# Kernel optimization log

Hardware: AMD Instinct MI355X
Metric: run time of the kernel (lower is better)

The kernel has to match this reference:

```python
import jax, jax.numpy as jnp
import numpy as np

N, E, ET, C, H, L = 100000, 500000, 3, 128, 128, 3
LN_EPS = 1e-5
L2_EPS = 1e-12


def setup_inputs() -> dict:
    ks = jax.random.split(jax.random.key(0), 12)
    s = 0.05
    return {
        "x": jax.random.normal(ks[0], (N, C), jnp.float32),
        "edges": jax.random.randint(ks[1], (ET, 2, E), 0, N),
        "Wp": jax.random.normal(ks[2], (ET, C, C), jnp.float32) * s,
        "bp": jax.random.normal(ks[3], (ET, C), jnp.float32) * s,
        "Wl0": jax.random.normal(ks[4], (ET, C, H), jnp.float32) * s,
        "bl0": jax.random.normal(ks[5], (ET, H), jnp.float32) * s,
        "Wr0": jax.random.normal(ks[6], (ET, C, H), jnp.float32) * s,
        "Wl": jax.random.normal(ks[7], (L - 1, ET, H, H), jnp.float32) * s,
        "bl": jax.random.normal(ks[8], (L - 1, ET, H), jnp.float32) * s,
        "Wr": jax.random.normal(ks[9], (L - 1, ET, H, H), jnp.float32) * s,
        "ln_g": jnp.ones((L - 1, H), jnp.float32),
        "ln_b": jnp.zeros((L - 1, H), jnp.float32),
    }


def _mean_aggr(msg, dst, n):
    # scatter-mean of per-edge messages onto destination nodes
    summed = jax.ops.segment_sum(msg, dst, num_segments=n)
    deg = jax.ops.segment_sum(jnp.ones((dst.shape[0],), msg.dtype), dst, num_segments=n)
    return summed / jnp.maximum(deg, 1.0)[:, None]


def _sage(h, ei, Wl_, bl_, Wr_, Wp_=None, bp_=None, normalize=False):
    # PyG SAGEConv: out = lin_l(mean_{j in N(i)} h_j) + lin_r(h_i)
    src, dst = ei[0], ei[1]
    hs = jax.nn.relu(h @ Wp_ + bp_) if Wp_ is not None else h  # project=True path
    agg = _mean_aggr(hs[src], dst, h.shape[0])
    out = agg @ Wl_ + bl_ + h @ Wr_
    if normalize:
        out = out / jnp.maximum(jnp.linalg.norm(out, axis=-1, keepdims=True), L2_EPS)
    return out


def _layer_norm(h, g, b):
    mu = h.mean(-1, keepdims=True)
    var = ((h - mu) ** 2).mean(-1, keepdims=True)
    return (h - mu) / jnp.sqrt(var + LN_EPS) * g + b


def _forward(x, edges, Wp, bp, Wl0, bl0, Wr0, Wl, bl, Wr, ln_g, ln_b):
    et = edges.shape[0]
    # layer 0: project=True, normalize=True; HeteroConv mean over edge types
    h = sum(_sage(x, edges[t], Wl0[t], bl0[t], Wr0[t], Wp[t], bp[t], True)
            for t in range(et)) / et
    h = _layer_norm(jax.nn.relu(h), ln_g[0], ln_b[0])  # dropout = identity (eval)
    n_rest = Wl.shape[0]
    for l in range(n_rest):
        h = sum(_sage(h, edges[t], Wl[l, t], bl[l, t], Wr[l, t])
                for t in range(et)) / et
        if l != n_rest - 1:
            h = _layer_norm(jax.nn.relu(h), ln_g[l + 1], ln_b[l + 1])
    return h


def reference(x, edges, Wp, bp, Wl0, bl0, Wr0, Wl, bl, Wr, ln_g, ln_b):
    return _forward(x, edges, Wp, bp, Wl0, bl0, Wr0, Wl, bl, Wr, ln_g, ln_b)
```

## Files before the change

### kernel.cpp

```cpp
#include <hip/hip_runtime.h>
#include <math.h>

#define CH 128
#define ETC 3
#define LN_EPS 1e-5f

typedef unsigned short u16;
typedef unsigned int u32;
typedef __attribute__((ext_vector_type(8))) short short8;
typedef __attribute__((ext_vector_type(4))) float f32x4;

__device__ __forceinline__ u16 f2bf(float f) {
    u32 u = __float_as_uint(f);
    u += 0x7FFFu + ((u >> 16) & 1u);
    return (u16)(u >> 16);
}
__device__ __forceinline__ float bflo(u32 u) { return __uint_as_float(u << 16); }
__device__ __forceinline__ float bfhi(u32 u) { return __uint_as_float(u & 0xFFFF0000u); }

__device__ __forceinline__ f32x4 mfma16(short8 a, short8 b, f32x4 c) {
    return __builtin_amdgcn_mfma_f32_16x16x32_bf16(a, b, c, 0, 0, 0);
}
__device__ __forceinline__ short8 ld8(const u16* p) { return *(const short8*)p; }

__global__ __launch_bounds__(256) void pack_w(
    const float* __restrict__ Wp, const float* __restrict__ Wl0,
    const float* __restrict__ Wr0, const float* __restrict__ Wl,
    const float* __restrict__ Wr, const float* __restrict__ bl,
    u16* __restrict__ Bswz, float* __restrict__ bls)
{
    if (blockIdx.x == 0) {
        int l = threadIdx.x >> 7, i = threadIdx.x & 127;
        bls[threadIdx.x] = (bl[((size_t)l * ETC + 0) * CH + i] +
                            bl[((size_t)l * ETC + 1) * CH + i] +
                            bl[((size_t)l * ETC + 2) * CH + i]) * (1.f / 3.f);
    }
    int grp = blockIdx.x * 256 + threadIdx.x;
    if (grp >= 17 * 2048) return;
    int lane = grp & 63;
    int t1 = grp >> 6;
    int nt = t1 & 7, t2 = t1 >> 3;
    int s = t2 & 3, mat = t2 >> 2;
    int q = lane >> 4, c = lane & 15;
    int nn = nt * 16 + c;

    const float* s0;
    const float* s1 = nullptr;
    const float* s2 = nullptr;
    float scale = 1.f;
    if (mat < 3) {
        s0 = Wp + (size_t)mat * CH * CH;
    } else if (mat < 9) {
        int t = (mat - 3) >> 1;
        s0 = ((mat - 3) & 1) ? Wr0 + (size_t)t * CH * CH : Wl0 + (size_t)t * CH * CH;
    } else {
        int l = (mat < 13) ? 0 : 1;
        int mm = mat - (l ? 13 : 9);
        scale = 1.f / 3.f;
        if (mm < 3) s0 = Wl + ((size_t)l * ETC + mm) * CH * CH;
        else {
            s0 = Wr + ((size_t)l * ETC + 0) * CH * CH;
            s1 = s0 + CH * CH;
            s2 = s1 + CH * CH;
        }
    }
    short8 o;
    #pragma unroll
    for (int j = 0; j < 8; ++j) {
        int k = s * 32 + q * 8 + j;
        float v = s0[(size_t)k * CH + nn];
        if (s1) v += s1[(size_t)k * CH + nn] + s2[(size_t)k * CH + nn];
        o[j] = (short)f2bf(v * scale);
    }
    *(short8*)&Bswz[(size_t)grp * 8] = o;
}

__global__ __launch_bounds__(256) void cast_x(
    const float* __restrict__ x, u16* __restrict__ xb, int total)
{
    int i = (blockIdx.x * 256 + threadIdx.x) * 8;
    if (i >= total) return;
    short8 o;
    #pragma unroll
    for (int j = 0; j < 8; ++j) o[j] = (short)f2bf(x[i + j]);
    *(short8*)&xb[i] = o;
}

template<int MODE>
__global__ __launch_bounds__(256, MODE == 0 ? 3 : 4) void combine_k(
    const u16* __restrict__ agg0, const u16* __restrict__ agg1,
    const u16* __restrict__ agg2, const u16* __restrict__ self,
    const u16* __restrict__ Bs, const float* __restrict__ bias,
    const float* __restrict__ lg, const float* __restrict__ lb,
    u16* __restrict__ outb, float* __restrict__ outf, int nrows)
{
    __shared__ __align__(16) u16 Bsh[CH * CH];
    const int tid = threadIdx.x;
    const int w = tid >> 6, lane = tid & 63;
    const int q = lane >> 4, c = lane & 15;
    const int rbase = (blockIdx.x * 4 + w) * 16;
    const int arow = rbase + c;
    constexpr int NM = (MODE == 0) ? 6 : ((MODE == 3) ? 1 : 4);
    constexpr int NA = (MODE == 3) ? 1 : 4;

    const u16* As[4];
    if constexpr (MODE == 3) {
        As[0] = self;
    } else {
        As[0] = agg0; As[1] = agg1; As[2] = agg2; As[3] = self;
    }

    short8 af[NA][4];
    #pragma unroll
    for (int a = 0; a < NA; ++a)
        #pragma unroll
        for (int s = 0; s < 4; ++s)
            af[a][s] = ld8(&As[a][(size_t)arow * CH + s * 32 + q * 8]);

    f32x4 acc[8] = {};
    f32x4 res[8] = {};

    #pragma unroll
    for (int m = 0; m < NM; ++m) {
        __syncthreads();
        const u16* bsrc = Bs + (size_t)m * CH * CH;
        #pragma unroll
        for (int i = 0; i < 8; ++i)
            *(short8*)&Bsh[(i * 256 + tid) * 8] = ld8(&bsrc[(i * 256 + tid) * 8]);
        __syncthreads();

        constexpr int AI_TBL0[6] = {0, 3, 1, 3, 2, 3};
        const int ai = (MODE == 0) ? AI_TBL0[m]
                     : (MODE == 3) ? 0
                     : ((m < 3) ? m : 3);

        #pragma unroll
        for (int s = 0; s < 4; ++s) {
            #pragma unroll
            for (int nt = 0; nt < 8; ++nt) {
                short8 bv = *(const short8*)&Bsh[((size_t)(s * 8 + nt) * 64 + lane) * 8];
                acc[nt] = mfma16(af[ai][s], bv, acc[nt]);
            }
        }

        if constexpr (MODE == 0) {
            if (m & 1) {
                const int t = m >> 1;
                float ss[4] = {0.f, 0.f, 0.f, 0.f};
                #pragma unroll
                for (int nt = 0; nt < 8; ++nt) {
                    float bf = bias[t * CH + nt * 16 + c];
                    #pragma unroll
                    for (int r = 0; r < 4; ++r) {
                        float v = acc[nt][r] + bf;
                        acc[nt][r] = v;
                        ss[r] += v * v;
                    }
                }
                #pragma unroll
                for (int msk = 1; msk < 16; msk <<= 1)
                    #pragma unroll
                    for (int r = 0; r < 4; ++r) ss[r] += __shfl_xor(ss[r], msk, 64);
                float sc[4];
                #pragma unroll
                for (int r = 0; r < 4; ++r)
                    sc[r] = 1.f / (3.f * fmaxf(sqrtf(ss[r]), 1e-12f));
                #pragma unroll
                for (int nt = 0; nt < 8; ++nt)
                    #pragma unroll
                    for (int r = 0; r < 4; ++r) {
                        res[nt][r] += acc[nt][r] * sc[r];
                        acc[nt][r] = 0.f;
                    }
            }
        }
    }

    if constexpr (MODE != 0) {
        #pragma unroll
        for (int nt = 0; nt < 8; ++nt) {
            float bv = bias[nt * 16 + c];
            #pragma unroll
            for (int r = 0; r < 4; ++r) res[nt][r] = acc[nt][r] + bv;
        }
    }

    if constexpr (MODE == 2) {
        #pragma unroll
        for (int nt = 0; nt < 8; ++nt)
            #pragma unroll
            for (int r = 0; r < 4; ++r) {
                int row = rbase + q * 4 + r;
                if (row < nrows) outf[(size_t)row * CH + nt * 16 + c] = res[nt][r];
            }
        return;
    }

    if constexpr (MODE == 3) {
        #pragma unroll
        for (int nt = 0; nt < 8; ++nt)
            #pragma unroll
            for (int r = 0; r < 4; ++r) {
                int row = rbase + q * 4 + r;
                outb[(size_t)row * CH + nt * 16 + c] = f2bf(fmaxf(res[nt][r], 0.f));
            }
        return;
    }

    {
        float s1[4] = {0.f, 0.f, 0.f, 0.f}, s2[4] = {0.f, 0.f, 0.f, 0.f};
        #pragma unroll
        for (int nt = 0; nt < 8; ++nt)
            #pragma unroll
            for (int r = 0; r < 4; ++r) {
                float v = fmaxf(res[nt][r], 0.f);
                res[nt][r] = v;
                s1[r] += v;
                s2[r] += v * v;
            }
        #pragma unroll
        for (int msk = 1; msk < 16; msk <<= 1)
            #pragma unroll
            for (int r = 0; r < 4; ++r) {
                s1[r] += __shfl_xor(s1[r], msk, 64);
                s2[r] += __shfl_xor(s2[r], msk, 64);
            }
        float mu[4], rs[4];
        #pragma unroll
        for (int r = 0; r < 4; ++r) {
            mu[r] = s1[r] * (1.f / 128.f);
            float var = s2[r] * (1.f / 128.f) - mu[r] * mu[r];
            rs[r] = rsqrtf(var + LN_EPS);
        }
        #pragma unroll
        for (int nt = 0; nt < 8; ++nt) {
            float gv = lg[nt * 16 + c], bv = lb[nt * 16 + c];
            #pragma unroll
            for (int r = 0; r < 4; ++r) {
                int row = rbase + q * 4 + r;
                outb[(size_t)row * CH + nt * 16 + c] =
                    f2bf((res[nt][r] - mu[r]) * rs[r] * gv + bv);
            }
        }
    }
}

__global__ __launch_bounds__(256) void agg_k(
    const u16* __restrict__ msg, const int* __restrict__ rowptr,
    const int* __restrict__ col, u16* __restrict__ agg, int n,
    int Ecap, unsigned long long aggstride)
{
    const int t = blockIdx.y;
    rowptr += (size_t)t * (n + 1);
    col += (size_t)t * Ecap;
    agg += (size_t)t * aggstride;

    int gid = blockIdx.x * 256 + threadIdx.x;
    int node = gid >> 5;
    int lane = threadIdx.x & 31;
    if (node >= n) return;
    int s = rowptr[node], e = rowptr[node + 1];
    const uint2* m64 = (const uint2*)msg;
    float a0 = 0.f, a1 = 0.f, a2 = 0.f, a3 = 0.f;
    float b0 = 0.f, b1 = 0.f, b2 = 0.f, b3 = 0.f;
    int j = s;
    for (; j + 2 <= e; j += 2) {
        int s0 = col[j], s1i = col[j + 1];
        uint2 v0 = m64[(size_t)s0 * 32 + lane];
        uint2 v1 = m64[(size_t)s1i * 32 + lane];
        a0 += bflo(v0.x); a1 += bfhi(v0.x); a2 += bflo(v0.y); a3 += bfhi(v0.y);
        b0 += bflo(v1.x); b1 += bfhi(v1.x); b2 += bflo(v1.y); b3 += bfhi(v1.y);
    }
    if (j < e) {
        int s0 = col[j];
        uint2 v0 = m64[(size_t)s0 * 32 + lane];
        a0 += bflo(v0.x); a1 += bfhi(v0.x); a2 += bflo(v0.y); a3 += bfhi(v0.y);
    }
    a0 += b0; a1 += b1; a2 += b2; a3 += b3;
    float inv = 1.f / (float)max(e - s, 1);
    uint2 o;
    o.x = (u32)f2bf(a0 * inv) | ((u32)f2bf(a1 * inv) << 16);
    o.y = (u32)f2bf(a2 * inv) | ((u32)f2bf(a3 * inv) << 16);
    ((uint2*)agg)[(size_t)node * 32 + lane] = o;
}

__global__ __launch_bounds__(256) void hist_k(
    const int* __restrict__ edges, int* __restrict__ cnt, int E, int n)
{
    int t = blockIdx.y;
    int e = blockIdx.x * 256 + threadIdx.x;
    if (e >= E) return;
    int dst = edges[(size_t)t * 2 * E + E + e];
    atomicAdd(&cnt[t * n + dst], 1);
}

__global__ __launch_bounds__(256) void scan1_k(
    const int* __restrict__ cnt, int* __restrict__ bsum, int n, int nbs)
{
    int t = blockIdx.y, b = blockIdx.x;
    int i = b * 256 + threadIdx.x;
    int v = (i < n) ? cnt[t * n + i] : 0;
    #pragma unroll
    for (int m = 1; m < 64; m <<= 1) v += __shfl_xor(v, m, 64);
    __shared__ int wsum[4];
    if ((threadIdx.x & 63) == 0) wsum[threadIdx.x >> 6] = v;
    __syncthreads();
    if (threadIdx.x == 0) bsum[t * nbs + b] = wsum[0] + wsum[1] + wsum[2] + wsum[3];
}

__global__ __launch_bounds__(512) void scan2_k(int* __restrict__ bsum, int nbs, int nb)
{
    int t = blockIdx.x;
    int tid = threadIdx.x;
    __shared__ int sh[512];
    int v = (tid < nb) ? bsum[t * nbs + tid] : 0;
    sh[tid] = v;
    __syncthreads();
    for (int off = 1; off < 512; off <<= 1) {
        int x = (tid >= off) ? sh[tid - off] : 0;
        __syncthreads();
        sh[tid] += x;
        __syncthreads();
    }
    if (tid < nb) bsum[t * nbs + tid] = sh[tid] - v;
}

__global__ __launch_bounds__(256) void scan3_k(
    const int* __restrict__ cnt, const int* __restrict__ bsum,
    int* __restrict__ rowptr, int n, int nbs)
{
    int t = blockIdx.y, b = blockIdx.x;
    int tid = threadIdx.x;
    int i = b * 256 + tid;
    __shared__ int sh[256];
    int v = (i < n) ? cnt[t * n + i] : 0;
    sh[tid] = v;
    __syncthreads();
    for (int off = 1; off < 256; off <<= 1) {
        int x = (tid >= off) ? sh[tid - off] : 0;
        __syncthreads();
        sh[tid] += x;
        __syncthreads();
    }
    int excl = sh[tid] - v + bsum[t * nbs + b];
    if (i < n) rowptr[(size_t)t * (n + 1) + i] = excl;
    if (i == n - 1) rowptr[(size_t)t * (n + 1) + n] = excl + v;
}

__global__ __launch_bounds__(256) void fill_k(
    const int* __restrict__ edges, const int* __restrict__ rowptr,
    int* __restrict__ cnt2, int* __restrict__ colbuf, int E, int n)
{
    int t = blockIdx.y;
    int e = blockIdx.x * 256 + threadIdx.x;
    if (e >= E) return;
    int src = edges[(size_t)t * 2 * E + e];
    int dst = edges[(size_t)t * 2 * E + E + e];
    int pos = rowptr[(size_t)t * (n + 1) + dst] + atomicAdd(&cnt2[t * n + dst], 1);
    colbuf[(size_t)t * E + pos] = src;
}

extern "C" void kernel_launch(void* const* d_in, const int* in_sizes, int n_in,
                              void* d_out, int out_size, void* d_ws, size_t ws_size,
                              hipStream_t stream) {
    const float* x    = (const float*)d_in[0];
    const int*   edges= (const int*)d_in[1];
    const float* Wp   = (const float*)d_in[2];
    const float* bp   = (const float*)d_in[3];
    const float* Wl0  = (const float*)d_in[4];
    const float* bl0  = (const float*)d_in[5];
    const float* Wr0  = (const float*)d_in[6];
    const float* Wl   = (const float*)d_in[7];
    const float* bl   = (const float*)d_in[8];
    const float* Wr   = (const float*)d_in[9];
    const float* ln_g = (const float*)d_in[10];
    const float* ln_b = (const float*)d_in[11];
    float* out = (float*)d_out;

    const int n  = in_sizes[0] / CH;
    const int E  = in_sizes[1] / (2 * ETC);
    const int npad = ((n + 255) / 256) * 256;
    const int NBS = 512;
    const int nb = (n + 255) / 256;
    const size_t MS = (size_t)CH * CH;

    char* p = (char*)d_ws;
    u16* xb   = (u16*)p;  p += (size_t)npad * CH * 2;
    u16* hs   = (u16*)p;  p += (size_t)npad * CH * 2;
    u16* agg  = (u16*)p;  p += (size_t)ETC * npad * CH * 2;
    u16* Bswz = (u16*)p;  p += 17 * MS * 2;
    float* bls = (float*)p; p += 256 * 4;
    int* cnt    = (int*)p;  p += (size_t)ETC * n * 4;
    int* rowptr = (int*)p;  p += (size_t)ETC * (n + 1) * 4;
    int* colbuf = (int*)p;  p += (size_t)ETC * E * 4;
    int* bsum   = (int*)p;

    const dim3 b256(256);
    const dim3 ge((E + 255) / 256, ETC);
    const dim3 gs(nb, ETC);
    const int gb = (n + 63) / 64;
    const int ga = (n * 32 + 255) / 256;

    hipMemsetAsync(cnt, 0, (size_t)ETC * n * sizeof(int), stream);
    hist_k<<<ge, b256, 0, stream>>>(edges, cnt, E, n);
    scan1_k<<<gs, b256, 0, stream>>>(cnt, bsum, n, NBS);
    scan2_k<<<ETC, 512, 0, stream>>>(bsum, NBS, nb);
    scan3_k<<<gs, b256, 0, stream>>>(cnt, bsum, rowptr, n, NBS);
    hipMemsetAsync(cnt, 0, (size_t)ETC * n * sizeof(int), stream);
    fill_k<<<ge, b256, 0, stream>>>(edges, rowptr, cnt, colbuf, E, n);

    pack_w<<<136, b256, 0, stream>>>(Wp, Wl0, Wr0, Wl, Wr, bl, Bswz, bls);
    cast_x<<<(n * CH / 8 + 255) / 256, b256, 0, stream>>>(x, xb, n * CH);

    for (int t = 0; t < ETC; ++t) {
        combine_k<3><<<gb, b256, 0, stream>>>(
            nullptr, nullptr, nullptr, xb, Bswz + (size_t)t * MS, bp + t * CH,
            nullptr, nullptr, hs, nullptr, n);
        agg_k<<<dim3(ga, 1), b256, 0, stream>>>(hs, rowptr + (size_t)t * (n + 1),
                                                colbuf + (size_t)t * E,
                                                agg + (size_t)t * npad * CH, n, 0, 0ull);
    }
    combine_k<0><<<gb, b256, 0, stream>>>(agg, agg + (size_t)npad * CH,
                                          agg + (size_t)2 * npad * CH, xb,
                                          Bswz + 3 * MS, bl0, ln_g, ln_b, hs, nullptr, n);

    agg_k<<<dim3(ga, ETC), b256, 0, stream>>>(hs, rowptr, colbuf, agg, n, E,
                                              (unsigned long long)npad * CH);
    combine_k<1><<<gb, b256, 0, stream>>>(agg, agg + (size_t)npad * CH,
                                          agg + (size_t)2 * npad * CH, hs,
                                          Bswz + 9 * MS, bls, ln_g + CH, ln_b + CH,
                                          hs, nullptr, n);

    agg_k<<<dim3(ga, ETC), b256, 0, stream>>>(hs, rowptr, colbuf, agg, n, E,
                                              (unsigned long long)npad * CH);
    combine_k<2><<<gb, b256, 0, stream>>>(agg, agg + (size_t)npad * CH,
                                          agg + (size_t)2 * npad * CH, hs,
                                          Bswz + 13 * MS, bls + CH, nullptr, nullptr,
                                          nullptr, out, n);
}
```

Baseline: 675.2 us.

## Widen aggregation loads to 16 lanes per node and bucket edges before CSR fill

The mean-aggregation kernel now gives each node 16 lanes that each load 128 bits, where it used 32 lanes loading 64 bits. The edge loop is unrolled by four gathers, and the sums go into packed float2 accumulators. The CSR build adds a coarse bucketing pass that groups edges by destination block of 128 nodes into a pair buffer placed in the agg workspace. The final fill then scatters with better locality for its atomics and colbuf writes. The cost is an extra kernel, a memset and one more pass over the edges in exchange for less random scatter traffic.

After: 873.0 us. 1.29x slower.

```diff
diff --git a/kernel.cpp b/kernel.cpp
--- a/kernel.cpp
+++ b/kernel.cpp
@@ -9,6 +9,7 @@
 typedef unsigned int u32;
 typedef __attribute__((ext_vector_type(8))) short short8;
 typedef __attribute__((ext_vector_type(4))) float f32x4;
+typedef __attribute__((ext_vector_type(2))) float f32x2;
 
 __device__ __forceinline__ u16 f2bf(float f) {
     u32 u = __float_as_uint(f);
@@ -245,6 +246,14 @@
     }
 }
 
+#define ACC4(v) do { \
+        f32x2 aa, bb; \
+        aa[0] = bflo((v).x); aa[1] = bflo((v).y); ev01 += aa; \
+        bb[0] = bfhi((v).x); bb[1] = bfhi((v).y); od01 += bb; \
+        aa[0] = bflo((v).z); aa[1] = bflo((v).w); ev23 += aa; \
+        bb[0] = bfhi((v).z); bb[1] = bfhi((v).w); od23 += bb; \
+    } while (0)
+
 __global__ __launch_bounds__(256) void agg_k(
     const u16* __restrict__ msg, const int* __restrict__ rowptr,
     const int* __restrict__ col, u16* __restrict__ agg, int n,
@@ -256,32 +265,35 @@
     agg += (size_t)t * aggstride;
 
     int gid = blockIdx.x * 256 + threadIdx.x;
-    int node = gid >> 5;
-    int lane = threadIdx.x & 31;
+    int node = gid >> 4;
+    int lane = threadIdx.x & 15;
     if (node >= n) return;
     int s = rowptr[node], e = rowptr[node + 1];
-    const uint2* m64 = (const uint2*)msg;
-    float a0 = 0.f, a1 = 0.f, a2 = 0.f, a3 = 0.f;
-    float b0 = 0.f, b1 = 0.f, b2 = 0.f, b3 = 0.f;
+    const uint4* m128 = (const uint4*)msg;
+
+    f32x2 ev01 = {0.f, 0.f}, ev23 = {0.f, 0.f};
+    f32x2 od01 = {0.f, 0.f}, od23 = {0.f, 0.f};
+
     int j = s;
-    for (; j + 2 <= e; j += 2) {
-        int s0 = col[j], s1i = col[j + 1];
-        uint2 v0 = m64[(size_t)s0 * 32 + lane];
-        uint2 v1 = m64[(size_t)s1i * 32 + lane];
-        a0 += bflo(v0.x); a1 += bfhi(v0.x); a2 += bflo(v0.y); a3 += bfhi(v0.y);
-        b0 += bflo(v1.x); b1 += bfhi(v1.x); b2 += bflo(v1.y); b3 += bfhi(v1.y);
-    }
-    if (j < e) {
-        int s0 = col[j];
-        uint2 v0 = m64[(size_t)s0 * 32 + lane];
-        a0 += bflo(v0.x); a1 += bfhi(v0.x); a2 += bflo(v0.y); a3 += bfhi(v0.y);
-    }
-    a0 += b0; a1 += b1; a2 += b2; a3 += b3;
+    for (; j + 4 <= e; j += 4) {
+        int c0 = col[j], c1 = col[j + 1], c2 = col[j + 2], c3 = col[j + 3];
+        uint4 v0 = m128[(size_t)c0 * 16 + lane];
+        uint4 v1 = m128[(size_t)c1 * 16 + lane];
+        uint4 v2 = m128[(size_t)c2 * 16 + lane];
+        uint4 v3 = m128[(size_t)c3 * 16 + lane];
+        ACC4(v0); ACC4(v1); ACC4(v2); ACC4(v3);
+    }
+    for (; j < e; ++j) {
+        uint4 v0 = m128[(size_t)col[j] * 16 + lane];
+        ACC4(v0);
+    }
     float inv = 1.f / (float)max(e - s, 1);
-    uint2 o;
-    o.x = (u32)f2bf(a0 * inv) | ((u32)f2bf(a1 * inv) << 16);
-    o.y = (u32)f2bf(a2 * inv) | ((u32)f2bf(a3 * inv) << 16);
-    ((uint2*)agg)[(size_t)node * 32 + lane] = o;
+    uint4 o;
+    o.x = (u32)f2bf(ev01[0] * inv) | ((u32)f2bf(od01[0] * inv) << 16);
+    o.y = (u32)f2bf(ev01[1] * inv) | ((u32)f2bf(od01[1] * inv) << 16);
+    o.z = (u32)f2bf(ev23[0] * inv) | ((u32)f2bf(od23[0] * inv) << 16);
+    o.w = (u32)f2bf(ev23[1] * inv) | ((u32)f2bf(od23[1] * inv) << 16);
+    ((uint4*)agg)[(size_t)node * 16 + lane] = o;
 }
 
 __global__ __launch_bounds__(256) void hist_k(
@@ -347,15 +359,30 @@
     if (i == n - 1) rowptr[(size_t)t * (n + 1) + n] = excl + v;
 }
 
-__global__ __launch_bounds__(256) void fill_k(
+__global__ __launch_bounds__(256) void bucket_k(
     const int* __restrict__ edges, const int* __restrict__ rowptr,
-    int* __restrict__ cnt2, int* __restrict__ colbuf, int E, int n)
+    int* __restrict__ bcur, uint2* __restrict__ pairbuf, int E, int n, int nbk)
 {
     int t = blockIdx.y;
     int e = blockIdx.x * 256 + threadIdx.x;
     if (e >= E) return;
     int src = edges[(size_t)t * 2 * E + e];
     int dst = edges[(size_t)t * 2 * E + E + e];
+    int b = dst >> 7;
+    int base = rowptr[(size_t)t * (n + 1) + ((size_t)b << 7)];
+    int pos = base + atomicAdd(&bcur[t * nbk + b], 1);
+    pairbuf[(size_t)t * E + pos] = make_uint2((u32)src, (u32)dst);
+}
+
+__global__ __launch_bounds__(256) void fill2_k(
+    const uint2* __restrict__ pairbuf, const int* __restrict__ rowptr,
+    int* __restrict__ cnt2, int* __restrict__ colbuf, int E, int n)
+{
+    int t = blockIdx.y;
+    int e = blockIdx.x * 256 + threadIdx.x;
+    if (e >= E) return;
+    uint2 p = pairbuf[(size_t)t * E + e];
+    int src = (int)p.x, dst = (int)p.y;
     int pos = rowptr[(size_t)t * (n + 1) + dst] + atomicAdd(&cnt2[t * n + dst], 1);
     colbuf[(size_t)t * E + pos] = src;
 }
@@ -382,6 +409,7 @@
     const int npad = ((n + 255) / 256) * 256;
     const int NBS = 512;
     const int nb = (n + 255) / 256;
+    const int nbk = (n + 127) / 128;
     const size_t MS = (size_t)CH * CH;
 
     char* p = (char*)d_ws;
@@ -393,13 +421,15 @@
     int* cnt    = (int*)p;  p += (size_t)ETC * n * 4;
     int* rowptr = (int*)p;  p += (size_t)ETC * (n + 1) * 4;
     int* colbuf = (int*)p;  p += (size_t)ETC * E * 4;
-    int* bsum   = (int*)p;
+    int* bsum   = (int*)p;  p += (size_t)ETC * NBS * 4;
+    int* bcur   = (int*)p;
+    uint2* pairbuf = (uint2*)agg;
 
     const dim3 b256(256);
     const dim3 ge((E + 255) / 256, ETC);
     const dim3 gs(nb, ETC);
     const int gb = (n + 63) / 64;
-    const int ga = (n * 32 + 255) / 256;
+    const int ga = (n * 16 + 255) / 256;
 
     hipMemsetAsync(cnt, 0, (size_t)ETC * n * sizeof(int), stream);
     hist_k<<<ge, b256, 0, stream>>>(edges, cnt, E, n);
@@ -407,7 +437,9 @@
     scan2_k<<<ETC, 512, 0, stream>>>(bsum, NBS, nb);
     scan3_k<<<gs, b256, 0, stream>>>(cnt, bsum, rowptr, n, NBS);
     hipMemsetAsync(cnt, 0, (size_t)ETC * n * sizeof(int), stream);
-    fill_k<<<ge, b256, 0, stream>>>(edges, rowptr, cnt, colbuf, E, n);
+    hipMemsetAsync(bcur, 0, (size_t)ETC * nbk * sizeof(int), stream);
+    bucket_k<<<ge, b256, 0, stream>>>(edges, rowptr, bcur, pairbuf, E, n, nbk);
+    fill2_k<<<ge, b256, 0, stream>>>(pairbuf, rowptr, cnt, colbuf, E, n);
 
     pack_w<<<136, b256, 0, stream>>>(Wp, Wl0, Wr0, Wl, Wr, bl, Bswz, bls);
     cast_x<<<(n * CH / 8 + 255) / 256, b256, 0, stream>>>(x, xb, n * CH);
```
